# Optimization experiments

Hardware: AMD Instinct MI355X
Metric: run time of the kernel (lower is better)

Reference implementation:

```python
import jax, jax.numpy as jnp
import numpy as np

EPS = 1e-6

def _feature_map(x):
    # elu_feature_map: elu(x) + 1
    return jax.nn.elu(x) + 1.0

def setup_inputs() -> dict:
    key = jax.random.key(0)
    ks = jax.random.split(key, 7)
    B, C, H, W = 4, 128, 32, 32
    s = 1.0 / np.sqrt(C)
    return {
        "feature": jax.random.normal(ks[0], (B, C, H, W), dtype=jnp.float32),
        "wq": jax.random.normal(ks[1], (C, C), dtype=jnp.float32) * s,
        "bq": jax.random.normal(ks[2], (C,), dtype=jnp.float32) * s,
        "wk": jax.random.normal(ks[3], (C, C), dtype=jnp.float32) * s,
        "bk": jax.random.normal(ks[4], (C,), dtype=jnp.float32) * s,
        "wv": jax.random.normal(ks[5], (C, C), dtype=jnp.float32) * s,
        "bv": jax.random.normal(ks[6], (C,), dtype=jnp.float32) * s,
    }

def reference(feature, wq, bq, wk, bk, wv, bv):
    B, C, H, W = feature.shape
    # flatten(2).transpose(1,2): (B, C, H*W) -> (B, N, C)
    x = feature.reshape(B, C, H * W).transpose(0, 2, 1)
    # torch Linear: x @ W.T + b
    query = x @ wq.T + bq
    key_p = x @ wk.T + bk
    value = x @ wv.T + bv
    Q = _feature_map(query)  # (B, N, C)
    K = _feature_map(key_p)  # (B, N, C)
    # state=None path: Si = 0 + K; Ri = 0 + outer(K, V)
    Si = K                                           # (B, N, C)
    Ri = jnp.einsum('bnc,bnm->bncm', K, value)       # (B, N, C, M)
    Z = 1.0 / (jnp.einsum('bnc,bnc->bn', Q, Si) + EPS)  # (B, N)
    RLSA = jnp.einsum('bnc,bncm,bn->bnm', Q, Ri, Z)  # (B, N, M)
    return (RLSA, Ri, Si)
```

## Files before the change

### kernel.cpp

```cpp
#include <hip/hip_runtime.h>
#include <math.h>

#define C 128
#define N 1024
#define EPS 1e-6f

#define TR 16
#define XS_STRIDE 20

__global__ __launch_bounds__(256) void qkv_kernel(
    const float* __restrict__ feat,
    const float* __restrict__ wq, const float* __restrict__ bq,
    const float* __restrict__ wk, const float* __restrict__ bk,
    const float* __restrict__ wv, const float* __restrict__ bv,
    float* __restrict__ out_rlsa, float* __restrict__ out_si,
    float* __restrict__ ws_v)
{
    __shared__ float xs[C * XS_STRIDE];
    __shared__ float sred[4][8];

    const int t    = threadIdx.x;
    const int c    = t & 127;
    const int half = t >> 7;
    const int row0 = blockIdx.x * TR;
    const int b    = row0 >> 10;
    const int n0   = row0 & 1023;

    {
        const float* fb = feat + (size_t)b * C * N;
        #pragma unroll
        for (int f = t; f < 512; f += 256) {
            int j = f >> 2, q = f & 3;
            float4 v = *(const float4*)(fb + (size_t)j * N + n0 + q * 4);
            *(float4*)&xs[j * XS_STRIDE + q * 4] = v;
        }
    }
    __syncthreads();

    float aq[8] = {0}, ak[8] = {0}, av[8] = {0};
    const float4* wq4 = (const float4*)(wq + c * C);
    const float4* wk4 = (const float4*)(wk + c * C);
    const float4* wv4 = (const float4*)(wv + c * C);
    const int xoff = half * 8;

    #pragma unroll 8
    for (int j4 = 0; j4 < 32; ++j4) {
        float4 q4 = wq4[j4];
        float4 k4 = wk4[j4];
        float4 v4 = wv4[j4];
        #pragma unroll
        for (int u = 0; u < 4; ++u) {
            const float* xr = &xs[(j4 * 4 + u) * XS_STRIDE + xoff];
            float4 xa = *(const float4*)(xr);
            float4 xb = *(const float4*)(xr + 4);
            float wqv = (u == 0) ? q4.x : (u == 1) ? q4.y : (u == 2) ? q4.z : q4.w;
            float wkv = (u == 0) ? k4.x : (u == 1) ? k4.y : (u == 2) ? k4.z : k4.w;
            float wvv = (u == 0) ? v4.x : (u == 1) ? v4.y : (u == 2) ? v4.z : v4.w;
            aq[0] += xa.x * wqv; aq[1] += xa.y * wqv; aq[2] += xa.z * wqv; aq[3] += xa.w * wqv;
            aq[4] += xb.x * wqv; aq[5] += xb.y * wqv; aq[6] += xb.z * wqv; aq[7] += xb.w * wqv;
            ak[0] += xa.x * wkv; ak[1] += xa.y * wkv; ak[2] += xa.z * wkv; ak[3] += xa.w * wkv;
            ak[4] += xb.x * wkv; ak[5] += xb.y * wkv; ak[6] += xb.z * wkv; ak[7] += xb.w * wkv;
            av[0] += xa.x * wvv; av[1] += xa.y * wvv; av[2] += xa.z * wvv; av[3] += xa.w * wvv;
            av[4] += xb.x * wvv; av[5] += xb.y * wvv; av[6] += xb.z * wvv; av[7] += xb.w * wvv;
        }
    }

    const float bqc = bq[c], bkc = bk[c], bvc = bv[c];
    float qf[8], kf[8], vf[8];
    #pragma unroll
    for (int i = 0; i < 8; ++i) {
        float q = aq[i] + bqc;
        float k = ak[i] + bkc;
        qf[i] = q > 0.f ? q + 1.f : expf(q);
        kf[i] = k > 0.f ? k + 1.f : expf(k);
        vf[i] = av[i] + bvc;
    }

    const int wave = t >> 6;
    const int lane = t & 63;
    #pragma unroll
    for (int i = 0; i < 8; ++i) {
        float p = qf[i] * kf[i];
        #pragma unroll
        for (int off = 32; off > 0; off >>= 1) p += __shfl_down(p, off, 64);
        if (lane == 0) sred[wave][i] = p;
    }
    __syncthreads();

    #pragma unroll
    for (int i = 0; i < 8; ++i) {
        float S = sred[half * 2][i] + sred[half * 2 + 1][i];
        float coef = S / (S + EPS);
        size_t ro = (size_t)(row0 + half * 8 + i) * C + c;
        out_si[ro]   = kf[i];
        out_rlsa[ro] = coef * vf[i];
        ws_v[ro]     = vf[i];
    }
}

#define BROWS 4

__global__ __launch_bounds__(256) void ri_kernel(
    const float* __restrict__ si, const float* __restrict__ ws_v,
    float* __restrict__ out_ri)
{
    __shared__ float ks[BROWS * C];
    __shared__ float vs[BROWS * C];

    const int t  = threadIdx.x;
    const int r0 = blockIdx.x * BROWS;

    #pragma unroll
    for (int idx = t; idx < BROWS * C; idx += 256) {
        int rr = idx >> 7, cc = idx & 127;
        ks[idx] = si[(size_t)(r0 + rr) * C + cc];
        vs[idx] = ws_v[(size_t)(r0 + rr) * C + cc];
    }
    __syncthreads();

    const float4* vs4 = (const float4*)vs;
    #pragma unroll
    for (int rr = 0; rr < BROWS; ++rr) {
        float4* ri4 = (float4*)(out_ri + (size_t)(r0 + rr) * C * C);
        const float* krow = ks + rr * C;
        const float4* vrow4 = vs4 + rr * 32;
        #pragma unroll
        for (int i = 0; i < 16; ++i) {
            int f4 = i * 256 + t;
            float kc = krow[f4 >> 5];
            float4 vv = vrow4[f4 & 31];
            ri4[f4] = make_float4(kc * vv.x, kc * vv.y, kc * vv.z, kc * vv.w);
        }
    }
}

extern "C" void kernel_launch(void* const* d_in, const int* in_sizes, int n_in,
                              void* d_out, int out_size, void* d_ws, size_t ws_size,
                              hipStream_t stream) {
    const float* feat = (const float*)d_in[0];
    const float* wq   = (const float*)d_in[1];
    const float* bq   = (const float*)d_in[2];
    const float* wk   = (const float*)d_in[3];
    const float* bk   = (const float*)d_in[4];
    const float* wv   = (const float*)d_in[5];
    const float* bv   = (const float*)d_in[6];

    float* out  = (float*)d_out;
    float* rlsa = out;
    float* ri   = out + (size_t)4 * 1024 * 128;
    float* si   = ri  + (size_t)4 * 1024 * 128 * 128;

    float* ws_v = (float*)d_ws;

    qkv_kernel<<<4096 / TR, 256, 0, stream>>>(feat, wq, bq, wk, bk, wv, bv,
                                              rlsa, si, ws_v);
    ri_kernel<<<4096 / BROWS, 256, 0, stream>>>(si, ws_v, ri);
}
```

Measured before the change: 296.2 us.

## Fuse QKV projection and Ri outer-product into one kernel with nontemporal stores

New measurement: 310.9 us. 5.0% more time.

```diff
diff --git a/kernel.cpp b/kernel.cpp
--- a/kernel.cpp
+++ b/kernel.cpp
@@ -4,20 +4,23 @@
 #define C 128
 #define N 1024
 #define EPS 1e-6f
+#define TR 8
+#define XSTRIDE 12
 
-#define TR 16
-#define XS_STRIDE 20
+typedef float f4 __attribute__((ext_vector_type(4)));
 
-__global__ __launch_bounds__(256) void qkv_kernel(
+__global__ __launch_bounds__(256) void rlsa_fused(
     const float* __restrict__ feat,
     const float* __restrict__ wq, const float* __restrict__ bq,
     const float* __restrict__ wk, const float* __restrict__ bk,
     const float* __restrict__ wv, const float* __restrict__ bv,
-    float* __restrict__ out_rlsa, float* __restrict__ out_si,
-    float* __restrict__ ws_v)
+    float* __restrict__ out_rlsa, float* __restrict__ out_ri,
+    float* __restrict__ out_si)
 {
-    __shared__ float xs[C * XS_STRIDE];
-    __shared__ float sred[4][8];
+    __shared__ __attribute__((aligned(16))) float xs[C * XSTRIDE];
+    __shared__ __attribute__((aligned(16))) float ks[TR * C];
+    __shared__ __attribute__((aligned(16))) float vs[TR * C];
+    __shared__ float sred[4][4];
 
     const int t    = threadIdx.x;
     const int c    = t & 127;
@@ -28,20 +31,17 @@
 
     {
         const float* fb = feat + (size_t)b * C * N;
-        #pragma unroll
-        for (int f = t; f < 512; f += 256) {
-            int j = f >> 2, q = f & 3;
-            float4 v = *(const float4*)(fb + (size_t)j * N + n0 + q * 4);
-            *(float4*)&xs[j * XS_STRIDE + q * 4] = v;
-        }
+        int j = t >> 1, q = t & 1;
+        float4 v = *(const float4*)(fb + (size_t)j * N + n0 + q * 4);
+        *(float4*)&xs[j * XSTRIDE + q * 4] = v;
     }
     __syncthreads();
 
-    float aq[8] = {0}, ak[8] = {0}, av[8] = {0};
+    float aq[4] = {0,0,0,0}, ak[4] = {0,0,0,0}, av[4] = {0,0,0,0};
     const float4* wq4 = (const float4*)(wq + c * C);
     const float4* wk4 = (const float4*)(wk + c * C);
     const float4* wv4 = (const float4*)(wv + c * C);
-    const int xoff = half * 8;
+    const int xoff = half * 4;
 
     #pragma unroll 8
     for (int j4 = 0; j4 < 32; ++j4) {
@@ -50,36 +50,33 @@
         float4 v4 = wv4[j4];
         #pragma unroll
         for (int u = 0; u < 4; ++u) {
-            const float* xr = &xs[(j4 * 4 + u) * XS_STRIDE + xoff];
-            float4 xa = *(const float4*)(xr);
-            float4 xb = *(const float4*)(xr + 4);
+            float4 xa = *(const float4*)&xs[(j4 * 4 + u) * XSTRIDE + xoff];
             float wqv = (u == 0) ? q4.x : (u == 1) ? q4.y : (u == 2) ? q4.z : q4.w;
             float wkv = (u == 0) ? k4.x : (u == 1) ? k4.y : (u == 2) ? k4.z : k4.w;
             float wvv = (u == 0) ? v4.x : (u == 1) ? v4.y : (u == 2) ? v4.z : v4.w;
             aq[0] += xa.x * wqv; aq[1] += xa.y * wqv; aq[2] += xa.z * wqv; aq[3] += xa.w * wqv;
-            aq[4] += xb.x * wqv; aq[5] += xb.y * wqv; aq[6] += xb.z * wqv; aq[7] += xb.w * wqv;
             ak[0] += xa.x * wkv; ak[1] += xa.y * wkv; ak[2] += xa.z * wkv; ak[3] += xa.w * wkv;
-            ak[4] += xb.x * wkv; ak[5] += xb.y * wkv; ak[6] += xb.z * wkv; ak[7] += xb.w * wkv;
             av[0] += xa.x * wvv; av[1] += xa.y * wvv; av[2] += xa.z * wvv; av[3] += xa.w * wvv;
-            av[4] += xb.x * wvv; av[5] += xb.y * wvv; av[6] += xb.z * wvv; av[7] += xb.w * wvv;
         }
     }
 
     const float bqc = bq[c], bkc = bk[c], bvc = bv[c];
-    float qf[8], kf[8], vf[8];
+    float qf[4], kf[4], vf[4];
     #pragma unroll
-    for (int i = 0; i < 8; ++i) {
+    for (int i = 0; i < 4; ++i) {
         float q = aq[i] + bqc;
         float k = ak[i] + bkc;
         qf[i] = q > 0.f ? q + 1.f : expf(q);
         kf[i] = k > 0.f ? k + 1.f : expf(k);
         vf[i] = av[i] + bvc;
+        ks[(half * 4 + i) * C + c] = kf[i];
+        vs[(half * 4 + i) * C + c] = vf[i];
     }
 
     const int wave = t >> 6;
     const int lane = t & 63;
     #pragma unroll
-    for (int i = 0; i < 8; ++i) {
+    for (int i = 0; i < 4; ++i) {
         float p = qf[i] * kf[i];
         #pragma unroll
         for (int off = 32; off > 0; off >>= 1) p += __shfl_down(p, off, 64);
@@ -88,48 +85,25 @@
     __syncthreads();
 
     #pragma unroll
-    for (int i = 0; i < 8; ++i) {
+    for (int i = 0; i < 4; ++i) {
         float S = sred[half * 2][i] + sred[half * 2 + 1][i];
         float coef = S / (S + EPS);
-        size_t ro = (size_t)(row0 + half * 8 + i) * C + c;
+        size_t ro = (size_t)(row0 + half * 4 + i) * C + c;
         out_si[ro]   = kf[i];
         out_rlsa[ro] = coef * vf[i];
-        ws_v[ro]     = vf[i];
     }
-}
 
-#define BROWS 4
-
-__global__ __launch_bounds__(256) void ri_kernel(
-    const float* __restrict__ si, const float* __restrict__ ws_v,
-    float* __restrict__ out_ri)
-{
-    __shared__ float ks[BROWS * C];
-    __shared__ float vs[BROWS * C];
-
-    const int t  = threadIdx.x;
-    const int r0 = blockIdx.x * BROWS;
-
+    const int mq = t & 31;
+    const int chi = t >> 5;
     #pragma unroll
-    for (int idx = t; idx < BROWS * C; idx += 256) {
-        int rr = idx >> 7, cc = idx & 127;
-        ks[idx] = si[(size_t)(r0 + rr) * C + cc];
-        vs[idx] = ws_v[(size_t)(r0 + rr) * C + cc];
-    }
-    __syncthreads();
-
-    const float4* vs4 = (const float4*)vs;
-    #pragma unroll
-    for (int rr = 0; rr < BROWS; ++rr) {
-        float4* ri4 = (float4*)(out_ri + (size_t)(r0 + rr) * C * C);
+    for (int rr = 0; rr < TR; ++rr) {
+        f4* rbase = (f4*)(out_ri + (size_t)(row0 + rr) * C * C);
         const float* krow = ks + rr * C;
-        const float4* vrow4 = vs4 + rr * 32;
+        f4 vv = ((const f4*)(vs + rr * C))[mq];
         #pragma unroll
         for (int i = 0; i < 16; ++i) {
-            int f4 = i * 256 + t;
-            float kc = krow[f4 >> 5];
-            float4 vv = vrow4[f4 & 31];
-            ri4[f4] = make_float4(kc * vv.x, kc * vv.y, kc * vv.z, kc * vv.w);
+            float kc = krow[i * 8 + chi];
+            __builtin_nontemporal_store(kc * vv, rbase + i * 256 + t);
         }
     }
 }
@@ -150,9 +124,6 @@
     float* ri   = out + (size_t)4 * 1024 * 128;
     float* si   = ri  + (size_t)4 * 1024 * 128 * 128;
 
-    float* ws_v = (float*)d_ws;
-
-    qkv_kernel<<<4096 / TR, 256, 0, stream>>>(feat, wq, bq, wk, bk, wv, bv,
-                                              rlsa, si, ws_v);
-    ri_kernel<<<4096 / BROWS, 256, 0, stream>>>(si, ws_v, ri);
+    rlsa_fused<<<4096 / TR, 256, 0, stream>>>(feat, wq, bq, wk, bk, wv, bv,
+                                              rlsa, ri, si);
 }
```
